# Kernel tuning notes

Hardware: AMD Instinct MI355X
Metric: run time of the kernel (lower is better)

The kernel has to match this reference:

```python
import jax, jax.numpy as jnp
import numpy as np

B, N_ATOMS, N_ALIGN = 65536, 128, 64


def setup_inputs() -> dict:
    key = jax.random.key(0)
    k1, k2 = jax.random.split(key)
    traj = jax.random.normal(k1, (B, N_ATOMS, 3), dtype=jnp.float32)
    ref_pos = jax.random.normal(k2, (N_ATOMS, 3), dtype=jnp.float32)
    align_idx = jnp.arange(N_ALIGN, dtype=jnp.int32)  # 0-based (ids - 1)
    return {"traj": traj, "ref_pos": ref_pos, "align_idx": align_idx}


def reference(traj, ref_pos, align_idx):
    # --- __init__: centered reference coordinates of alignment atoms ---
    ref_x = ref_pos[align_idx]                      # [K, 3]
    ref_x = ref_x - jnp.mean(ref_x, axis=0)         # center

    # --- forward: Kabsch alignment per frame ---
    sel = traj[:, align_idx, :]                     # [B, K, 3]
    x_c = jnp.mean(sel, axis=1, keepdims=True)      # [B, 1, 3]
    x_notran = sel - x_c                            # [B, K, 3]
    # xtmp = x_notran^T  -> prod[b] = x_notran[b]^T @ ref_x : [B, 3, 3]
    prod = jnp.einsum('bki,kj->bij', x_notran, ref_x)

    u, s, vh = jnp.linalg.svd(prod)                 # u,vh: [B, 3, 3]
    sign_vec = jnp.sign(jnp.linalg.det(u @ vh))     # [B]
    # diag(1, 1, sign) applied on the right of u
    d = jnp.stack([jnp.ones_like(sign_vec), jnp.ones_like(sign_vec), sign_vec], axis=-1)
    rotate_mat = (u * d[:, None, :]) @ vh           # [B, 3, 3]

    aligned_traj = jnp.matmul(traj - x_c, rotate_mat)  # [B, N, 3]
    return aligned_traj
```

## Files before the change

### kernel.cpp

```cpp
#include <hip/hip_runtime.h>
#include <math.h>

#define NATOMS 128
#define NALIGN 64
#define FPB    8
#define TPB    256

#define JACOBI_ROT(app, aqq, apq, arp, arq, pcol, qcol)                 \
  {                                                                     \
    float _apq = (apq);                                                 \
    float _den = 2.0f * _apq;                                           \
    _den = copysignf(fmaxf(fabsf(_den), 1e-30f), _den);                 \
    float _tau = ((aqq) - (app)) / _den;                                \
    float _t = (_tau >= 0.0f ? 1.0f : -1.0f) /                          \
               (fabsf(_tau) + sqrtf(1.0f + _tau * _tau));               \
    float _c = rsqrtf(1.0f + _t * _t);                                  \
    float _s = _t * _c;                                                 \
    (app) -= _t * _apq;                                                 \
    (aqq) += _t * _apq;                                                 \
    (apq) = 0.0f;                                                      \
    float _rp = (arp), _rq = (arq);                                     \
    (arp) = _c * _rp - _s * _rq;                                        \
    (arq) = _s * _rp + _c * _rq;                                        \
    _Pragma("unroll")                                                   \
    for (int _r = 0; _r < 3; _r++) {                                    \
      float _vp = v[3 * _r + (pcol)], _vq = v[3 * _r + (qcol)];         \
      v[3 * _r + (pcol)] = _c * _vp - _s * _vq;                         \
      v[3 * _r + (qcol)] = _s * _vp + _c * _vq;                         \
    }                                                                   \
  }

__global__ __launch_bounds__(TPB) void align_kernel(
    const float* __restrict__ traj,
    const float* __restrict__ ref_pos,
    const int* __restrict__ align_idx,
    float* __restrict__ out,
    int B)
{
    __shared__ float4 s_rmap[NATOMS];

    const int t  = threadIdx.x;
    const int f0 = blockIdx.x * FPB;
    const int f  = t >> 5;
    const int r  = t & 31;
    const int gf = f0 + f;
    const bool valid = (gf < B);

    float4 q0, q1, q2;
    if (valid) {
        const float* p = traj + (size_t)gf * (NATOMS * 3) + r * 12;
        q0 = *(const float4*)(p);
        q1 = *(const float4*)(p + 4);
        q2 = *(const float4*)(p + 8);
    } else {
        q0 = q1 = q2 = make_float4(0.f, 0.f, 0.f, 0.f);
    }

    if (t < NALIGN) {
        const float4 z4 = make_float4(0.f, 0.f, 0.f, 0.f);
        s_rmap[t]          = z4;
        s_rmap[t + NALIGN] = z4;

        int idx = align_idx[t];
        float rx = ref_pos[idx * 3 + 0];
        float ry = ref_pos[idx * 3 + 1];
        float rz = ref_pos[idx * 3 + 2];
        float sx = rx, sy = ry, sz = rz;
        #pragma unroll
        for (int off = 32; off >= 1; off >>= 1) {
            sx += __shfl_xor(sx, off);
            sy += __shfl_xor(sy, off);
            sz += __shfl_xor(sz, off);
        }
        const float inv = 1.0f / (float)NALIGN;
        int slot = ((idx & 3) << 5) | (idx >> 2);
        s_rmap[slot] = make_float4(rx - sx * inv, ry - sy * inv, rz - sz * inv, 1.0f);
    }
    __syncthreads();

    float xx[4] = { q0.x, q0.w, q1.z, q2.y };
    float yy[4] = { q0.y, q1.x, q1.w, q2.z };
    float zz[4] = { q0.z, q1.y, q2.x, q2.w };

    float sx = 0.f, sy = 0.f, sz = 0.f;
    float c[9] = {0.f,0.f,0.f,0.f,0.f,0.f,0.f,0.f,0.f};
    #pragma unroll
    for (int j = 0; j < 4; j++) {
        float4 rm = s_rmap[(j << 5) | r];
        sx += rm.w * xx[j]; sy += rm.w * yy[j]; sz += rm.w * zz[j];
        c[0] += xx[j]*rm.x; c[1] += xx[j]*rm.y; c[2] += xx[j]*rm.z;
        c[3] += yy[j]*rm.x; c[4] += yy[j]*rm.y; c[5] += yy[j]*rm.z;
        c[6] += zz[j]*rm.x; c[7] += zz[j]*rm.y; c[8] += zz[j]*rm.z;
    }
    #pragma unroll
    for (int off = 16; off >= 1; off >>= 1) {
        sx += __shfl_xor(sx, off);
        sy += __shfl_xor(sy, off);
        sz += __shfl_xor(sz, off);
        #pragma unroll
        for (int jj = 0; jj < 9; jj++) c[jj] += __shfl_xor(c[jj], off);
    }
    const float invA = 1.0f / (float)NALIGN;
    const float xcx = sx * invA, xcy = sy * invA, xcz = sz * invA;

    const float* m = c;

    float a00 = m[0]*m[0] + m[3]*m[3] + m[6]*m[6];
    float a01 = m[0]*m[1] + m[3]*m[4] + m[6]*m[7];
    float a02 = m[0]*m[2] + m[3]*m[5] + m[6]*m[8];
    float a11 = m[1]*m[1] + m[4]*m[4] + m[7]*m[7];
    float a12 = m[1]*m[2] + m[4]*m[5] + m[7]*m[8];
    float a22 = m[2]*m[2] + m[5]*m[5] + m[8]*m[8];

    float v[9] = {1.f,0.f,0.f, 0.f,1.f,0.f, 0.f,0.f,1.f};
    #pragma unroll
    for (int sweep = 0; sweep < 5; sweep++) {
        JACOBI_ROT(a00, a11, a01, a02, a12, 0, 1);
        JACOBI_ROT(a00, a22, a02, a01, a12, 0, 2);
        JACOBI_ROT(a11, a22, a12, a01, a02, 1, 2);
    }

    float dd[3] = {a00, a11, a22};
    #pragma unroll
    for (int pass = 0; pass < 3; pass++) {
        const int ii = (pass == 2) ? 1 : 0;
        const int jj = (pass == 0) ? 1 : 2;
        float di = dd[ii], dj = dd[jj];
        bool sw = di < dj;
        dd[ii] = sw ? dj : di;
        dd[jj] = sw ? di : dj;
        #pragma unroll
        for (int rr = 0; rr < 3; rr++) {
            float a = v[3*rr+ii], b = v[3*rr+jj];
            v[3*rr+ii] = sw ? b : a;
            v[3*rr+jj] = sw ? a : b;
        }
    }

    float v0x = v[0], v0y = v[3], v0z = v[6];
    float v1x = v[1], v1y = v[4], v1z = v[7];
    float v2x = v[2], v2y = v[5], v2z = v[8];

    float u1x = m[0]*v0x + m[1]*v0y + m[2]*v0z;
    float u1y = m[3]*v0x + m[4]*v0y + m[5]*v0z;
    float u1z = m[6]*v0x + m[7]*v0y + m[8]*v0z;
    float n1 = rsqrtf(fmaxf(u1x*u1x + u1y*u1y + u1z*u1z, 1e-30f));
    u1x *= n1; u1y *= n1; u1z *= n1;

    float u2x = m[0]*v1x + m[1]*v1y + m[2]*v1z;
    float u2y = m[3]*v1x + m[4]*v1y + m[5]*v1z;
    float u2z = m[6]*v1x + m[7]*v1y + m[8]*v1z;
    float d12 = u1x*u2x + u1y*u2y + u1z*u2z;
    u2x -= d12 * u1x; u2y -= d12 * u1y; u2z -= d12 * u1z;
    float n2 = rsqrtf(fmaxf(u2x*u2x + u2y*u2y + u2z*u2z, 1e-30f));
    u2x *= n2; u2y *= n2; u2z *= n2;

    float u3x = u1y*u2z - u1z*u2y;
    float u3y = u1z*u2x - u1x*u2z;
    float u3z = u1x*u2y - u1y*u2x;
    float cxv = v1y*v2z - v1z*v2y;
    float cyv = v1z*v2x - v1x*v2z;
    float czv = v1x*v2y - v1y*v2x;
    float detv = v0x*cxv + v0y*cyv + v0z*czv;
    float sg = (detv >= 0.f) ? 1.f : -1.f;
    u3x *= sg; u3y *= sg; u3z *= sg;

    float R0 = u1x*v0x + u2x*v1x + u3x*v2x;
    float R1 = u1x*v0y + u2x*v1y + u3x*v2y;
    float R2 = u1x*v0z + u2x*v1z + u3x*v2z;
    float R3 = u1y*v0x + u2y*v1x + u3y*v2x;
    float R4 = u1y*v0y + u2y*v1y + u3y*v2y;
    float R5 = u1y*v0z + u2y*v1z + u3y*v2z;
    float R6 = u1z*v0x + u2z*v1x + u3z*v2x;
    float R7 = u1z*v0y + u2z*v1y + u3z*v2y;
    float R8 = u1z*v0z + u2z*v1z + u3z*v2z;

    if (valid) {
        float ox[4], oy[4], oz[4];
        #pragma unroll
        for (int j = 0; j < 4; j++) {
            float dx = xx[j] - xcx, dy = yy[j] - xcy, dz = zz[j] - xcz;
            ox[j] = dx*R0 + dy*R3 + dz*R6;
            oy[j] = dx*R1 + dy*R4 + dz*R7;
            oz[j] = dx*R2 + dy*R5 + dz*R8;
        }

        float* po = out + (size_t)gf * (NATOMS * 3) + r * 12;
        *(float4*)(po)     = make_float4(ox[0], oy[0], oz[0], ox[1]);
        *(float4*)(po + 4) = make_float4(oy[1], oz[1], ox[2], oy[2]);
        *(float4*)(po + 8) = make_float4(oz[2], ox[3], oy[3], oz[3]);
    }
}

extern "C" void kernel_launch(void* const* d_in, const int* in_sizes, int n_in,
                              void* d_out, int out_size, void* d_ws, size_t ws_size,
                              hipStream_t stream) {
    const float* traj      = (const float*)d_in[0];
    const float* ref_pos   = (const float*)d_in[1];
    const int*   align_idx = (const int*)d_in[2];
    float*       out       = (float*)d_out;

    int B = in_sizes[0] / (NATOMS * 3);
    int grid = (B + FPB - 1) / FPB;
    align_kernel<<<grid, TPB, 0, stream>>>(traj, ref_pos, align_idx, out, B);
}
```

Baseline: 215.2 us.

## Compute per-frame SVD once per frame via shared memory, 16 threads per frame

Each frame is now handled by 16 threads instead of 32, with each thread holding 8 atoms. Instead of every lane redundantly running the Jacobi eigensolver, one thread per frame solves it and shares the rotation and centroid through shared memory. This removes redundant ALU work and halves the shuffle-reduction depth. In exchange it adds two block barriers, serializes the solve onto 32 threads while the rest of the block idles, and raises per-thread register use.

```diff
diff --git a/kernel.cpp b/kernel.cpp
--- a/kernel.cpp
+++ b/kernel.cpp
@@ -3,8 +3,9 @@
 
 #define NATOMS 128
 #define NALIGN 64
-#define FPB    8
-#define TPB    256
+#define FPB    32
+#define TPF    16
+#define TPB    (FPB * TPF)
 
 #define JACOBI_ROT(app, aqq, apq, arp, arq, pcol, qcol)                 \
   {                                                                     \
@@ -18,7 +19,7 @@
     float _s = _t * _c;                                                 \
     (app) -= _t * _apq;                                                 \
     (aqq) += _t * _apq;                                                 \
-    (apq) = 0.0f;                                                      \
+    (apq) = 0.0f;                                                       \
     float _rp = (arp), _rq = (arq);                                     \
     (arp) = _c * _rp - _s * _rq;                                        \
     (arq) = _s * _rp + _c * _rq;                                        \
@@ -38,22 +39,29 @@
     int B)
 {
     __shared__ float4 s_rmap[NATOMS];
-
-    const int t  = threadIdx.x;
-    const int f0 = blockIdx.x * FPB;
-    const int f  = t >> 5;
-    const int r  = t & 31;
-    const int gf = f0 + f;
+    __shared__ float s_cov[FPB][13];
+
+    const int t   = threadIdx.x;
+    const int f   = t >> 4;
+    const int sub = t & 15;
+    const int gf  = blockIdx.x * FPB + f;
     const bool valid = (gf < B);
 
-    float4 q0, q1, q2;
+    float x[8], y[8], z[8];
     if (valid) {
-        const float* p = traj + (size_t)gf * (NATOMS * 3) + r * 12;
-        q0 = *(const float4*)(p);
-        q1 = *(const float4*)(p + 4);
-        q2 = *(const float4*)(p + 8);
+        const float4* p = (const float4*)(traj + (size_t)gf * (NATOMS * 3) + sub * 24);
+        float4 q0 = p[0], q1 = p[1], q2 = p[2], q3 = p[3], q4 = p[4], q5 = p[5];
+        x[0]=q0.x; y[0]=q0.y; z[0]=q0.z;
+        x[1]=q0.w; y[1]=q1.x; z[1]=q1.y;
+        x[2]=q1.z; y[2]=q1.w; z[2]=q2.x;
+        x[3]=q2.y; y[3]=q2.z; z[3]=q2.w;
+        x[4]=q3.x; y[4]=q3.y; z[4]=q3.z;
+        x[5]=q3.w; y[5]=q4.x; z[5]=q4.y;
+        x[6]=q4.z; y[6]=q4.w; z[6]=q5.x;
+        x[7]=q5.y; y[7]=q5.z; z[7]=q5.w;
     } else {
-        q0 = q1 = q2 = make_float4(0.f, 0.f, 0.f, 0.f);
+        #pragma unroll
+        for (int j = 0; j < 8; j++) { x[j]=0.f; y[j]=0.f; z[j]=0.f; }
     }
 
     if (t < NALIGN) {
@@ -73,122 +81,140 @@
             sz += __shfl_xor(sz, off);
         }
         const float inv = 1.0f / (float)NALIGN;
-        int slot = ((idx & 3) << 5) | (idx >> 2);
+        int slot = ((idx & 7) << 4) | (idx >> 3);
         s_rmap[slot] = make_float4(rx - sx * inv, ry - sy * inv, rz - sz * inv, 1.0f);
     }
     __syncthreads();
 
-    float xx[4] = { q0.x, q0.w, q1.z, q2.y };
-    float yy[4] = { q0.y, q1.x, q1.w, q2.z };
-    float zz[4] = { q0.z, q1.y, q2.x, q2.w };
-
-    float sx = 0.f, sy = 0.f, sz = 0.f;
-    float c[9] = {0.f,0.f,0.f,0.f,0.f,0.f,0.f,0.f,0.f};
-    #pragma unroll
-    for (int j = 0; j < 4; j++) {
-        float4 rm = s_rmap[(j << 5) | r];
-        sx += rm.w * xx[j]; sy += rm.w * yy[j]; sz += rm.w * zz[j];
-        c[0] += xx[j]*rm.x; c[1] += xx[j]*rm.y; c[2] += xx[j]*rm.z;
-        c[3] += yy[j]*rm.x; c[4] += yy[j]*rm.y; c[5] += yy[j]*rm.z;
-        c[6] += zz[j]*rm.x; c[7] += zz[j]*rm.y; c[8] += zz[j]*rm.z;
-    }
-    #pragma unroll
-    for (int off = 16; off >= 1; off >>= 1) {
-        sx += __shfl_xor(sx, off);
-        sy += __shfl_xor(sy, off);
-        sz += __shfl_xor(sz, off);
-        #pragma unroll
-        for (int jj = 0; jj < 9; jj++) c[jj] += __shfl_xor(c[jj], off);
-    }
-    const float invA = 1.0f / (float)NALIGN;
-    const float xcx = sx * invA, xcy = sy * invA, xcz = sz * invA;
-
-    const float* m = c;
-
-    float a00 = m[0]*m[0] + m[3]*m[3] + m[6]*m[6];
-    float a01 = m[0]*m[1] + m[3]*m[4] + m[6]*m[7];
-    float a02 = m[0]*m[2] + m[3]*m[5] + m[6]*m[8];
-    float a11 = m[1]*m[1] + m[4]*m[4] + m[7]*m[7];
-    float a12 = m[1]*m[2] + m[4]*m[5] + m[7]*m[8];
-    float a22 = m[2]*m[2] + m[5]*m[5] + m[8]*m[8];
-
-    float v[9] = {1.f,0.f,0.f, 0.f,1.f,0.f, 0.f,0.f,1.f};
-    #pragma unroll
-    for (int sweep = 0; sweep < 5; sweep++) {
-        JACOBI_ROT(a00, a11, a01, a02, a12, 0, 1);
-        JACOBI_ROT(a00, a22, a02, a01, a12, 0, 2);
-        JACOBI_ROT(a11, a22, a12, a01, a02, 1, 2);
-    }
-
-    float dd[3] = {a00, a11, a22};
-    #pragma unroll
-    for (int pass = 0; pass < 3; pass++) {
-        const int ii = (pass == 2) ? 1 : 0;
-        const int jj = (pass == 0) ? 1 : 2;
-        float di = dd[ii], dj = dd[jj];
-        bool sw = di < dj;
-        dd[ii] = sw ? dj : di;
-        dd[jj] = sw ? di : dj;
-        #pragma unroll
-        for (int rr = 0; rr < 3; rr++) {
-            float a = v[3*rr+ii], b = v[3*rr+jj];
-            v[3*rr+ii] = sw ? b : a;
-            v[3*rr+jj] = sw ? a : b;
-        }
-    }
-
-    float v0x = v[0], v0y = v[3], v0z = v[6];
-    float v1x = v[1], v1y = v[4], v1z = v[7];
-    float v2x = v[2], v2y = v[5], v2z = v[8];
-
-    float u1x = m[0]*v0x + m[1]*v0y + m[2]*v0z;
-    float u1y = m[3]*v0x + m[4]*v0y + m[5]*v0z;
-    float u1z = m[6]*v0x + m[7]*v0y + m[8]*v0z;
-    float n1 = rsqrtf(fmaxf(u1x*u1x + u1y*u1y + u1z*u1z, 1e-30f));
-    u1x *= n1; u1y *= n1; u1z *= n1;
-
-    float u2x = m[0]*v1x + m[1]*v1y + m[2]*v1z;
-    float u2y = m[3]*v1x + m[4]*v1y + m[5]*v1z;
-    float u2z = m[6]*v1x + m[7]*v1y + m[8]*v1z;
-    float d12 = u1x*u2x + u1y*u2y + u1z*u2z;
-    u2x -= d12 * u1x; u2y -= d12 * u1y; u2z -= d12 * u1z;
-    float n2 = rsqrtf(fmaxf(u2x*u2x + u2y*u2y + u2z*u2z, 1e-30f));
-    u2x *= n2; u2y *= n2; u2z *= n2;
-
-    float u3x = u1y*u2z - u1z*u2y;
-    float u3y = u1z*u2x - u1x*u2z;
-    float u3z = u1x*u2y - u1y*u2x;
-    float cxv = v1y*v2z - v1z*v2y;
-    float cyv = v1z*v2x - v1x*v2z;
-    float czv = v1x*v2y - v1y*v2x;
-    float detv = v0x*cxv + v0y*cyv + v0z*czv;
-    float sg = (detv >= 0.f) ? 1.f : -1.f;
-    u3x *= sg; u3y *= sg; u3z *= sg;
-
-    float R0 = u1x*v0x + u2x*v1x + u3x*v2x;
-    float R1 = u1x*v0y + u2x*v1y + u3x*v2y;
-    float R2 = u1x*v0z + u2x*v1z + u3x*v2z;
-    float R3 = u1y*v0x + u2y*v1x + u3y*v2x;
-    float R4 = u1y*v0y + u2y*v1y + u3y*v2y;
-    float R5 = u1y*v0z + u2y*v1z + u3y*v2z;
-    float R6 = u1z*v0x + u2z*v1x + u3z*v2x;
-    float R7 = u1z*v0y + u2z*v1y + u3z*v2y;
-    float R8 = u1z*v0z + u2z*v1z + u3z*v2z;
+    {
+        float sx = 0.f, sy = 0.f, sz = 0.f;
+        float c[9] = {0.f,0.f,0.f,0.f,0.f,0.f,0.f,0.f,0.f};
+        #pragma unroll
+        for (int j = 0; j < 8; j++) {
+            float4 rm = s_rmap[(j << 4) | sub];
+            sx += rm.w * x[j]; sy += rm.w * y[j]; sz += rm.w * z[j];
+            c[0] += x[j]*rm.x; c[1] += x[j]*rm.y; c[2] += x[j]*rm.z;
+            c[3] += y[j]*rm.x; c[4] += y[j]*rm.y; c[5] += y[j]*rm.z;
+            c[6] += z[j]*rm.x; c[7] += z[j]*rm.y; c[8] += z[j]*rm.z;
+        }
+        #pragma unroll
+        for (int off = 8; off >= 1; off >>= 1) {
+            sx += __shfl_xor(sx, off);
+            sy += __shfl_xor(sy, off);
+            sz += __shfl_xor(sz, off);
+            #pragma unroll
+            for (int jj = 0; jj < 9; jj++) c[jj] += __shfl_xor(c[jj], off);
+        }
+        if (sub == 0) {
+            #pragma unroll
+            for (int jj = 0; jj < 9; jj++) s_cov[f][jj] = c[jj];
+            const float inv = 1.0f / (float)NALIGN;
+            s_cov[f][9]  = sx * inv;
+            s_cov[f][10] = sy * inv;
+            s_cov[f][11] = sz * inv;
+        }
+    }
+    __syncthreads();
+
+    if (t < FPB) {
+        float m[9];
+        #pragma unroll
+        for (int j = 0; j < 9; j++) m[j] = s_cov[t][j];
+
+        float a00 = m[0]*m[0] + m[3]*m[3] + m[6]*m[6];
+        float a01 = m[0]*m[1] + m[3]*m[4] + m[6]*m[7];
+        float a02 = m[0]*m[2] + m[3]*m[5] + m[6]*m[8];
+        float a11 = m[1]*m[1] + m[4]*m[4] + m[7]*m[7];
+        float a12 = m[1]*m[2] + m[4]*m[5] + m[7]*m[8];
+        float a22 = m[2]*m[2] + m[5]*m[5] + m[8]*m[8];
+
+        float v[9] = {1.f,0.f,0.f, 0.f,1.f,0.f, 0.f,0.f,1.f};
+        #pragma unroll
+        for (int sweep = 0; sweep < 5; sweep++) {
+            JACOBI_ROT(a00, a11, a01, a02, a12, 0, 1);
+            JACOBI_ROT(a00, a22, a02, a01, a12, 0, 2);
+            JACOBI_ROT(a11, a22, a12, a01, a02, 1, 2);
+        }
+
+        float dd[3] = {a00, a11, a22};
+        #pragma unroll
+        for (int pass = 0; pass < 3; pass++) {
+            const int ii = (pass == 2) ? 1 : 0;
+            const int jj = (pass == 0) ? 1 : 2;
+            float di = dd[ii], dj = dd[jj];
+            bool sw = di < dj;
+            dd[ii] = sw ? dj : di;
+            dd[jj] = sw ? di : dj;
+            #pragma unroll
+            for (int rr = 0; rr < 3; rr++) {
+                float a = v[3*rr+ii], b = v[3*rr+jj];
+                v[3*rr+ii] = sw ? b : a;
+                v[3*rr+jj] = sw ? a : b;
+            }
+        }
+
+        float v0x = v[0], v0y = v[3], v0z = v[6];
+        float v1x = v[1], v1y = v[4], v1z = v[7];
+        float v2x = v[2], v2y = v[5], v2z = v[8];
+
+        float u1x = m[0]*v0x + m[1]*v0y + m[2]*v0z;
+        float u1y = m[3]*v0x + m[4]*v0y + m[5]*v0z;
+        float u1z = m[6]*v0x + m[7]*v0y + m[8]*v0z;
+        float n1 = rsqrtf(fmaxf(u1x*u1x + u1y*u1y + u1z*u1z, 1e-30f));
+        u1x *= n1; u1y *= n1; u1z *= n1;
+
+        float u2x = m[0]*v1x + m[1]*v1y + m[2]*v1z;
+        float u2y = m[3]*v1x + m[4]*v1y + m[5]*v1z;
+        float u2z = m[6]*v1x + m[7]*v1y + m[8]*v1z;
+        float d12 = u1x*u2x + u1y*u2y + u1z*u2z;
+        u2x -= d12 * u1x; u2y -= d12 * u1y; u2z -= d12 * u1z;
+        float n2 = rsqrtf(fmaxf(u2x*u2x + u2y*u2y + u2z*u2z, 1e-30f));
+        u2x *= n2; u2y *= n2; u2z *= n2;
+
+        float u3x = u1y*u2z - u1z*u2y;
+        float u3y = u1z*u2x - u1x*u2z;
+        float u3z = u1x*u2y - u1y*u2x;
+        float cxv = v1y*v2z - v1z*v2y;
+        float cyv = v1z*v2x - v1x*v2z;
+        float czv = v1x*v2y - v1y*v2x;
+        float detv = v0x*cxv + v0y*cyv + v0z*czv;
+        float sg = (detv >= 0.f) ? 1.f : -1.f;
+        u3x *= sg; u3y *= sg; u3z *= sg;
+
+        s_cov[t][0] = u1x*v0x + u2x*v1x + u3x*v2x;
+        s_cov[t][1] = u1x*v0y + u2x*v1y + u3x*v2y;
+        s_cov[t][2] = u1x*v0z + u2x*v1z + u3x*v2z;
+        s_cov[t][3] = u1y*v0x + u2y*v1x + u3y*v2x;
+        s_cov[t][4] = u1y*v0y + u2y*v1y + u3y*v2y;
+        s_cov[t][5] = u1y*v0z + u2y*v1z + u3y*v2z;
+        s_cov[t][6] = u1z*v0x + u2z*v1x + u3z*v2x;
+        s_cov[t][7] = u1z*v0y + u2z*v1y + u3z*v2y;
+        s_cov[t][8] = u1z*v0z + u2z*v1z + u3z*v2z;
+    }
+    __syncthreads();
 
     if (valid) {
-        float ox[4], oy[4], oz[4];
-        #pragma unroll
-        for (int j = 0; j < 4; j++) {
-            float dx = xx[j] - xcx, dy = yy[j] - xcy, dz = zz[j] - xcz;
+        float R0 = s_cov[f][0], R1 = s_cov[f][1], R2 = s_cov[f][2];
+        float R3 = s_cov[f][3], R4 = s_cov[f][4], R5 = s_cov[f][5];
+        float R6 = s_cov[f][6], R7 = s_cov[f][7], R8 = s_cov[f][8];
+        float xcx = s_cov[f][9], xcy = s_cov[f][10], xcz = s_cov[f][11];
+
+        float ox[8], oy[8], oz[8];
+        #pragma unroll
+        for (int j = 0; j < 8; j++) {
+            float dx = x[j] - xcx, dy = y[j] - xcy, dz = z[j] - xcz;
             ox[j] = dx*R0 + dy*R3 + dz*R6;
             oy[j] = dx*R1 + dy*R4 + dz*R7;
             oz[j] = dx*R2 + dy*R5 + dz*R8;
         }
 
-        float* po = out + (size_t)gf * (NATOMS * 3) + r * 12;
-        *(float4*)(po)     = make_float4(ox[0], oy[0], oz[0], ox[1]);
-        *(float4*)(po + 4) = make_float4(oy[1], oz[1], ox[2], oy[2]);
-        *(float4*)(po + 8) = make_float4(oz[2], ox[3], oy[3], oz[3]);
+        float4* po = (float4*)(out + (size_t)gf * (NATOMS * 3) + sub * 24);
+        po[0] = make_float4(ox[0], oy[0], oz[0], ox[1]);
+        po[1] = make_float4(oy[1], oz[1], ox[2], oy[2]);
+        po[2] = make_float4(oz[2], ox[3], oy[3], oz[3]);
+        po[3] = make_float4(ox[4], oy[4], oz[4], ox[5]);
+        po[4] = make_float4(oy[5], oz[5], ox[6], oy[6]);
+        po[5] = make_float4(oz[6], ox[7], oy[7], oz[7]);
     }
 }
 
```

Measured after the change: 198.3 us. 1.08x faster.

## Stage frames through swizzled LDS for coalesced I/O and centralize SVD per frame

Applied to the files above, without the earlier changes.

Global loads and stores now go through a per-wavefront shared-memory staging buffer, so each 64-lane wavefront reads and writes contiguous float4s covering two frames. The buffer uses an XOR-swizzled layout to avoid bank conflicts. The per-frame 3x3 SVD/Jacobi, previously repeated redundantly by all 32 lanes of each frame, is now computed once per frame by a single thread, and the rotation and centroid are broadcast through shared memory. This adds extra block-wide barriers, and the SVD runs serially on only 16 threads, which could leave the block idle during that phase.

```diff
diff --git a/kernel.cpp b/kernel.cpp
--- a/kernel.cpp
+++ b/kernel.cpp
@@ -3,8 +3,10 @@
 
 #define NATOMS 128
 #define NALIGN 64
-#define FPB    8
-#define TPB    256
+#define WPB    8
+#define FPW    2
+#define FPB    (WPB * FPW)
+#define TPB    (WPB * 64)
 
 #define JACOBI_ROT(app, aqq, apq, arp, arq, pcol, qcol)                 \
   {                                                                     \
@@ -18,7 +20,7 @@
     float _s = _t * _c;                                                 \
     (app) -= _t * _apq;                                                 \
     (aqq) += _t * _apq;                                                 \
-    (apq) = 0.0f;                                                      \
+    (apq) = 0.0f;                                                       \
     float _rp = (arp), _rq = (arq);                                     \
     (arp) = _c * _rp - _s * _rq;                                        \
     (arq) = _s * _rp + _c * _rq;                                        \
@@ -30,81 +32,8 @@
     }                                                                   \
   }
 
-__global__ __launch_bounds__(TPB) void align_kernel(
-    const float* __restrict__ traj,
-    const float* __restrict__ ref_pos,
-    const int* __restrict__ align_idx,
-    float* __restrict__ out,
-    int B)
+__device__ __forceinline__ void svd_rotation(const float* m, float* R)
 {
-    __shared__ float4 s_rmap[NATOMS];
-
-    const int t  = threadIdx.x;
-    const int f0 = blockIdx.x * FPB;
-    const int f  = t >> 5;
-    const int r  = t & 31;
-    const int gf = f0 + f;
-    const bool valid = (gf < B);
-
-    float4 q0, q1, q2;
-    if (valid) {
-        const float* p = traj + (size_t)gf * (NATOMS * 3) + r * 12;
-        q0 = *(const float4*)(p);
-        q1 = *(const float4*)(p + 4);
-        q2 = *(const float4*)(p + 8);
-    } else {
-        q0 = q1 = q2 = make_float4(0.f, 0.f, 0.f, 0.f);
-    }
-
-    if (t < NALIGN) {
-        const float4 z4 = make_float4(0.f, 0.f, 0.f, 0.f);
-        s_rmap[t]          = z4;
-        s_rmap[t + NALIGN] = z4;
-
-        int idx = align_idx[t];
-        float rx = ref_pos[idx * 3 + 0];
-        float ry = ref_pos[idx * 3 + 1];
-        float rz = ref_pos[idx * 3 + 2];
-        float sx = rx, sy = ry, sz = rz;
-        #pragma unroll
-        for (int off = 32; off >= 1; off >>= 1) {
-            sx += __shfl_xor(sx, off);
-            sy += __shfl_xor(sy, off);
-            sz += __shfl_xor(sz, off);
-        }
-        const float inv = 1.0f / (float)NALIGN;
-        int slot = ((idx & 3) << 5) | (idx >> 2);
-        s_rmap[slot] = make_float4(rx - sx * inv, ry - sy * inv, rz - sz * inv, 1.0f);
-    }
-    __syncthreads();
-
-    float xx[4] = { q0.x, q0.w, q1.z, q2.y };
-    float yy[4] = { q0.y, q1.x, q1.w, q2.z };
-    float zz[4] = { q0.z, q1.y, q2.x, q2.w };
-
-    float sx = 0.f, sy = 0.f, sz = 0.f;
-    float c[9] = {0.f,0.f,0.f,0.f,0.f,0.f,0.f,0.f,0.f};
-    #pragma unroll
-    for (int j = 0; j < 4; j++) {
-        float4 rm = s_rmap[(j << 5) | r];
-        sx += rm.w * xx[j]; sy += rm.w * yy[j]; sz += rm.w * zz[j];
-        c[0] += xx[j]*rm.x; c[1] += xx[j]*rm.y; c[2] += xx[j]*rm.z;
-        c[3] += yy[j]*rm.x; c[4] += yy[j]*rm.y; c[5] += yy[j]*rm.z;
-        c[6] += zz[j]*rm.x; c[7] += zz[j]*rm.y; c[8] += zz[j]*rm.z;
-    }
-    #pragma unroll
-    for (int off = 16; off >= 1; off >>= 1) {
-        sx += __shfl_xor(sx, off);
-        sy += __shfl_xor(sy, off);
-        sz += __shfl_xor(sz, off);
-        #pragma unroll
-        for (int jj = 0; jj < 9; jj++) c[jj] += __shfl_xor(c[jj], off);
-    }
-    const float invA = 1.0f / (float)NALIGN;
-    const float xcx = sx * invA, xcy = sy * invA, xcz = sz * invA;
-
-    const float* m = c;
-
     float a00 = m[0]*m[0] + m[3]*m[3] + m[6]*m[6];
     float a01 = m[0]*m[1] + m[3]*m[4] + m[6]*m[7];
     float a02 = m[0]*m[2] + m[3]*m[5] + m[6]*m[8];
@@ -165,30 +94,158 @@
     float sg = (detv >= 0.f) ? 1.f : -1.f;
     u3x *= sg; u3y *= sg; u3z *= sg;
 
-    float R0 = u1x*v0x + u2x*v1x + u3x*v2x;
-    float R1 = u1x*v0y + u2x*v1y + u3x*v2y;
-    float R2 = u1x*v0z + u2x*v1z + u3x*v2z;
-    float R3 = u1y*v0x + u2y*v1x + u3y*v2x;
-    float R4 = u1y*v0y + u2y*v1y + u3y*v2y;
-    float R5 = u1y*v0z + u2y*v1z + u3y*v2z;
-    float R6 = u1z*v0x + u2z*v1x + u3z*v2x;
-    float R7 = u1z*v0y + u2z*v1y + u3z*v2y;
-    float R8 = u1z*v0z + u2z*v1z + u3z*v2z;
-
-    if (valid) {
+    R[0] = u1x*v0x + u2x*v1x + u3x*v2x;
+    R[1] = u1x*v0y + u2x*v1y + u3x*v2y;
+    R[2] = u1x*v0z + u2x*v1z + u3x*v2z;
+    R[3] = u1y*v0x + u2y*v1x + u3y*v2x;
+    R[4] = u1y*v0y + u2y*v1y + u3y*v2y;
+    R[5] = u1y*v0z + u2y*v1z + u3y*v2z;
+    R[6] = u1z*v0x + u2z*v1x + u3z*v2x;
+    R[7] = u1z*v0y + u2z*v1y + u3z*v2y;
+    R[8] = u1z*v0z + u2z*v1z + u3z*v2z;
+}
+
+__device__ __forceinline__ int slotAddr(int o, int so) {
+    return (o << 6) | ((so << 4) ^ ((o & 6) << 3));
+}
+
+__global__ __launch_bounds__(TPB) void align_kernel(
+    const float* __restrict__ traj,
+    const float* __restrict__ ref_pos,
+    const int* __restrict__ align_idx,
+    float* __restrict__ out,
+    int B)
+{
+    __shared__ float4 s_rmap[NATOMS];
+    __shared__ __align__(16) float s_stage[WPB][1024];
+    __shared__ float s_cov[FPB][13];
+
+    const int t = threadIdx.x;
+    const int w = t >> 6;
+    const int l = t & 63;
+    const int chunk0 = blockIdx.x * FPB + w * FPW;
+    const int lim = B * 96;
+
+    const float4* __restrict__ gin = (const float4*)traj;
+    char* wst = (char*)&s_stage[w][0];
+
+    float4 st[3];
+    #pragma unroll
+    for (int c = 0; c < 3; c++) {
+        int gq = chunk0 * 96 + c * 64 + l;
+        st[c] = (gq < lim) ? gin[gq] : make_float4(0.f, 0.f, 0.f, 0.f);
+    }
+
+    if (t < NALIGN) {
+        const float4 z4 = make_float4(0.f, 0.f, 0.f, 0.f);
+        s_rmap[t]          = z4;
+        s_rmap[t + NALIGN] = z4;
+        int idx = align_idx[t];
+        float rx = ref_pos[idx * 3 + 0];
+        float ry = ref_pos[idx * 3 + 1];
+        float rz = ref_pos[idx * 3 + 2];
+        float sx = rx, sy = ry, sz = rz;
+        #pragma unroll
+        for (int off = 32; off >= 1; off >>= 1) {
+            sx += __shfl_xor(sx, off);
+            sy += __shfl_xor(sy, off);
+            sz += __shfl_xor(sz, off);
+        }
+        const float inv = 1.0f / (float)NALIGN;
+        int slot = ((idx & 3) << 5) | (idx >> 2);
+        s_rmap[slot] = make_float4(rx - sx*inv, ry - sy*inv, rz - sz*inv, 1.0f);
+    }
+
+    #pragma unroll
+    for (int c = 0; c < 3; c++) {
+        int q  = c * 64 + l;
+        int o  = q / 3;
+        int so = q - 3 * o;
+        *(float4*)(wst + slotAddr(o, so)) = st[c];
+    }
+    __syncthreads();
+
+    float4 u0 = *(const float4*)(wst + slotAddr(l, 0));
+    float4 u1 = *(const float4*)(wst + slotAddr(l, 1));
+    float4 u2 = *(const float4*)(wst + slotAddr(l, 2));
+    float x[4] = { u0.x, u0.w, u1.z, u2.y };
+    float y[4] = { u0.y, u1.x, u1.w, u2.z };
+    float z[4] = { u0.z, u1.y, u2.x, u2.w };
+
+    const int lf = l & 31;
+    {
+        float sx = 0.f, sy = 0.f, sz = 0.f;
+        float c9[9] = {0.f,0.f,0.f,0.f,0.f,0.f,0.f,0.f,0.f};
+        #pragma unroll
+        for (int j = 0; j < 4; j++) {
+            float4 rm = s_rmap[(j << 5) | lf];
+            sx += rm.w * x[j]; sy += rm.w * y[j]; sz += rm.w * z[j];
+            c9[0] += x[j]*rm.x; c9[1] += x[j]*rm.y; c9[2] += x[j]*rm.z;
+            c9[3] += y[j]*rm.x; c9[4] += y[j]*rm.y; c9[5] += y[j]*rm.z;
+            c9[6] += z[j]*rm.x; c9[7] += z[j]*rm.y; c9[8] += z[j]*rm.z;
+        }
+        #pragma unroll
+        for (int off = 16; off >= 1; off >>= 1) {
+            sx += __shfl_xor(sx, off);
+            sy += __shfl_xor(sy, off);
+            sz += __shfl_xor(sz, off);
+            #pragma unroll
+            for (int jj = 0; jj < 9; jj++) c9[jj] += __shfl_xor(c9[jj], off);
+        }
+        if (lf == 0) {
+            int fi = w * FPW + (l >> 5);
+            #pragma unroll
+            for (int jj = 0; jj < 9; jj++) s_cov[fi][jj] = c9[jj];
+            const float inv = 1.0f / (float)NALIGN;
+            s_cov[fi][9]  = sx * inv;
+            s_cov[fi][10] = sy * inv;
+            s_cov[fi][11] = sz * inv;
+        }
+    }
+    __syncthreads();
+
+    if (t < FPB && (blockIdx.x * FPB + t) < B) {
+        float m[9];
+        #pragma unroll
+        for (int j = 0; j < 9; j++) m[j] = s_cov[t][j];
+        float R[9];
+        svd_rotation(m, R);
+        #pragma unroll
+        for (int j = 0; j < 9; j++) s_cov[t][j] = R[j];
+    }
+    __syncthreads();
+
+    {
+        const int fi = w * FPW + (l >> 5);
+        float R0 = s_cov[fi][0], R1 = s_cov[fi][1], R2 = s_cov[fi][2];
+        float R3 = s_cov[fi][3], R4 = s_cov[fi][4], R5 = s_cov[fi][5];
+        float R6 = s_cov[fi][6], R7 = s_cov[fi][7], R8 = s_cov[fi][8];
+        float xcx = s_cov[fi][9], xcy = s_cov[fi][10], xcz = s_cov[fi][11];
+
         float ox[4], oy[4], oz[4];
         #pragma unroll
         for (int j = 0; j < 4; j++) {
-            float dx = xx[j] - xcx, dy = yy[j] - xcy, dz = zz[j] - xcz;
+            float dx = x[j] - xcx, dy = y[j] - xcy, dz = z[j] - xcz;
             ox[j] = dx*R0 + dy*R3 + dz*R6;
             oy[j] = dx*R1 + dy*R4 + dz*R7;
             oz[j] = dx*R2 + dy*R5 + dz*R8;
         }
 
-        float* po = out + (size_t)gf * (NATOMS * 3) + r * 12;
-        *(float4*)(po)     = make_float4(ox[0], oy[0], oz[0], ox[1]);
-        *(float4*)(po + 4) = make_float4(oy[1], oz[1], ox[2], oy[2]);
-        *(float4*)(po + 8) = make_float4(oz[2], ox[3], oy[3], oz[3]);
+        *(float4*)(wst + slotAddr(l, 0)) = make_float4(ox[0], oy[0], oz[0], ox[1]);
+        *(float4*)(wst + slotAddr(l, 1)) = make_float4(oy[1], oz[1], ox[2], oy[2]);
+        *(float4*)(wst + slotAddr(l, 2)) = make_float4(oz[2], ox[3], oy[3], oz[3]);
+    }
+    __syncthreads();
+
+    float4* __restrict__ gout = (float4*)out;
+    #pragma unroll
+    for (int c = 0; c < 3; c++) {
+        int q  = c * 64 + l;
+        int o  = q / 3;
+        int so = q - 3 * o;
+        float4 v4 = *(const float4*)(wst + slotAddr(o, so));
+        int gq = chunk0 * 96 + q;
+        if (gq < lim) gout[gq] = v4;
     }
 }
 
```

Result: faster. 195.3 us (-9.2%).
